# Kernel optimization log

Measured on AMD Instinct MI355X. Metric: run time of the kernel, lower is better.

## Reference

```python
import jax, jax.numpy as jnp
import numpy as np

N_MASTER = 100000
N_BOND = 200000
N_GLOB = 5000
E1 = 400000
E2 = 100000
D_IN = 64
D_OUT = 64
H = 4
SLOPE = 0.2  # leaky relu negative slope


def _mlp(x, W0, b0, W1, b1, W2):
    # LinearN with num_fc_layers=3: ELU, ELU, Identity (last layer no bias)
    h = jax.nn.elu(x @ W0 + b0)
    h = jax.nn.elu(h @ W1 + b1)
    return h @ W2  # (N, H*D_OUT)


def setup_inputs() -> dict:
    key = jax.random.key(0)
    ks = jax.random.split(key, 32)
    s = 0.1  # weight scale
    d = {
        "master_feats": jax.random.normal(ks[0], (N_MASTER, D_IN), jnp.float32),
        "bond_feats": jax.random.normal(ks[1], (N_BOND, D_IN), jnp.float32),
        "global_feats": jax.random.normal(ks[2], (N_GLOB, D_IN), jnp.float32),
        "atom_W0": jax.random.normal(ks[3], (D_IN, D_OUT), jnp.float32) * s,
        "atom_b0": jnp.zeros((D_OUT,), jnp.float32),
        "atom_W1": jax.random.normal(ks[4], (D_OUT, D_OUT), jnp.float32) * s,
        "atom_b1": jnp.zeros((D_OUT,), jnp.float32),
        "atom_W2": jax.random.normal(ks[5], (D_OUT, H * D_OUT), jnp.float32) * s,
        "bond_W0": jax.random.normal(ks[6], (D_IN, D_OUT), jnp.float32) * s,
        "bond_b0": jnp.zeros((D_OUT,), jnp.float32),
        "bond_W1": jax.random.normal(ks[7], (D_OUT, D_OUT), jnp.float32) * s,
        "bond_b1": jnp.zeros((D_OUT,), jnp.float32),
        "bond_W2": jax.random.normal(ks[8], (D_OUT, H * D_OUT), jnp.float32) * s,
        "glob_W0": jax.random.normal(ks[9], (D_IN, D_OUT), jnp.float32) * s,
        "glob_b0": jnp.zeros((D_OUT,), jnp.float32),
        "glob_W1": jax.random.normal(ks[10], (D_OUT, D_OUT), jnp.float32) * s,
        "glob_b1": jnp.zeros((D_OUT,), jnp.float32),
        "glob_W2": jax.random.normal(ks[11], (D_OUT, H * D_OUT), jnp.float32) * s,
        "attn_l": jax.random.normal(ks[12], (H, D_OUT), jnp.float32) * s,
        "attn_r": jax.random.normal(ks[13], (H, D_OUT), jnp.float32) * s,
        "e1_src": jax.random.randint(ks[14], (E1,), 0, N_BOND, jnp.int32),
        "e1_dst": jax.random.randint(ks[15], (E1,), 0, N_MASTER, jnp.int32),
        "e2_src": jax.random.randint(ks[16], (E2,), 0, N_GLOB, jnp.int32),
        "e2_dst": jax.random.randint(ks[17], (E2,), 0, N_MASTER, jnp.int32),
    }
    return d


def reference(master_feats, bond_feats, global_feats,
              atom_W0, atom_b0, atom_W1, atom_b1, atom_W2,
              bond_W0, bond_b0, bond_W1, bond_b1, bond_W2,
              glob_W0, glob_b0, glob_W1, glob_b1, glob_W2,
              attn_l, attn_r, e1_src, e1_dst, e2_src, e2_dst):
    # Per-node-type projections to (N, H, D_OUT)
    ft_m = _mlp(master_feats, atom_W0, atom_b0, atom_W1, atom_b1, atom_W2).reshape(N_MASTER, H, D_OUT)
    ft_b = _mlp(bond_feats, bond_W0, bond_b0, bond_W1, bond_b1, bond_W2).reshape(N_BOND, H, D_OUT)
    ft_g = _mlp(global_feats, glob_W0, glob_b0, glob_W1, glob_b1, glob_W2).reshape(N_GLOB, H, D_OUT)

    er = jnp.einsum('nhd,hd->nh', ft_m, attn_r)  # master (dst) scores
    el_b = jnp.einsum('nhd,hd->nh', ft_b, attn_l)
    el_g = jnp.einsum('nhd,hd->nh', ft_g, attn_l)

    # Per-edge logits: u_add_v then leaky relu
    e1 = jax.nn.leaky_relu(el_b[e1_src] + er[e1_dst], negative_slope=SLOPE)  # (E1, H)
    e2 = jax.nn.leaky_relu(el_g[e2_src] + er[e2_dst], negative_slope=SLOPE)  # (E2, H)

    # Joint edge softmax over all incoming edges per master node
    dst_all = jnp.concatenate([e1_dst, e2_dst])  # (E1+E2,)
    e_all = jnp.concatenate([e1, e2], axis=0)    # (E1+E2, H)
    emax = jax.ops.segment_max(e_all, dst_all, num_segments=N_MASTER)  # (N, H)
    ex = jnp.exp(e_all - emax[dst_all])
    esum = jax.ops.segment_sum(ex, dst_all, num_segments=N_MASTER)     # (N, H)
    a = ex / esum[dst_all]                                             # (E, H)

    # Aggregate: u_mul_e, sum per destination master node
    src_ft = jnp.concatenate([ft_b[e1_src], ft_g[e2_src]], axis=0)     # (E, H, D)
    msgs = src_ft * a[:, :, None]
    rst = jax.ops.segment_sum(msgs, dst_all, num_segments=N_MASTER)    # (N, H, D)
    return rst
```

## Files before the change

### kernel.cpp

```cpp
#include <hip/hip_runtime.h>

#define NM 100000
#define NB 200000
#define NG 5000
#define NE1 400000
#define NE2 100000
#define NE (NE1 + NE2)
#define NMP 100004
#define SCAN_BLOCKS 391

typedef __attribute__((ext_vector_type(8))) short bf16x8;
typedef __attribute__((ext_vector_type(4))) short short4v;
typedef __attribute__((ext_vector_type(4))) float f32x4;

__device__ __forceinline__ unsigned short f2bf(float f) {
    unsigned int u = __float_as_uint(f);
    u += 0x7FFFu + ((u >> 16) & 1u);
    return (unsigned short)(u >> 16);
}
__device__ __forceinline__ float bf2f(unsigned short u) {
    return __uint_as_float((unsigned int)u << 16);
}
__device__ __forceinline__ float elu_f(float x) {
    return x > 0.f ? x : __expf(x) - 1.f;
}
__device__ __forceinline__ char* swz(char* base, int j, int byteoff) {
    return base + j * 128 + ((((byteoff >> 4) ^ (j & 7)) << 4) | (byteoff & 15));
}

struct WEnt { const float* W; short* o; int I; int off; };
struct WAll { WEnt e[6]; };

__global__ __launch_bounds__(256) void wprep_all_kernel(WAll a)
{
    const int idx = blockIdx.x * 256 + threadIdx.x;
    #pragma unroll
    for (int j = 5; j >= 0; --j) {
        if (idx >= a.e[j].off) {
            const int local = idx - a.e[j].off;
            const int I = a.e[j].I;
            const int i = local >> 6, k = local & 63;
            a.e[j].o[local] = (short)f2bf(a.e[j].W[k * I + i]);
            break;
        }
    }
}

__global__ __launch_bounds__(256) void wt2prep_kernel(
    const float* __restrict__ W2b, const float* __restrict__ W2g,
    short* __restrict__ wt2)
{
    const int idx = blockIdx.x * 256 + threadIdx.x;
    const int i = idx >> 7, k = idx & 127;
    const float v = (k < 64) ? W2b[(k << 8) + i] : W2g[((k - 64) << 8) + i];
    wt2[idx] = (short)f2bf(v);
}

struct Eff3 { const float* W2[3]; const float* attn[3]; float* eff[3]; };
__global__ __launch_bounds__(256) void eff3_kernel(Eff3 a)
{
    const int b = blockIdx.x;
    const int t = threadIdx.x;
    const int h = t >> 6, k = t & 63;
    const float* wrow = a.W2[b] + (k << 8) + (h << 6);
    const float* arow = a.attn[b] + (h << 6);
    float s = 0.f;
    #pragma unroll 8
    for (int d = 0; d < 64; ++d) s = fmaf(wrow[d], arow[d], s);
    a.eff[b][(h << 6) + k] = s;
}

struct MlpArgs {
    const float* x[3]; int N[3];
    const short* W0t[3]; const float* b0[3];
    const short* W1t[3]; const float* b1[3];
    const float* eff[3];
    float* score[3];
    unsigned short* h2o[3];
    int bstart[3];
};

__global__ __launch_bounds__(256, 4) void mlp2_all_kernel(MlpArgs A)
{
    __shared__ __attribute__((aligned(128))) char ldsA[64 * 128];
    __shared__ __attribute__((aligned(128))) char ldsB[64 * 128];

    const int which = (blockIdx.x >= (unsigned)A.bstart[2]) ? 2
                    : (blockIdx.x >= (unsigned)A.bstart[1]) ? 1 : 0;
    const float* x = A.x[which];
    const int N = A.N[which];
    const short* W0t = A.W0t[which];
    const float* b0p = A.b0[which];
    const short* W1t = A.W1t[which];
    const float* b1p = A.b1[which];
    const float* eff = A.eff[which];
    float* score = A.score[which];
    unsigned short* h2p = A.h2o[which];

    const int tid = threadIdx.x;
    const int w = tid >> 6, l = tid & 63;
    const int g = l >> 4, c = l & 15;
    const int r0 = (blockIdx.x - A.bstart[which]) << 6;

    {
        const int j = tid >> 2, q = tid & 3;
        const int row = r0 + j;
        bf16x8 o0 = (bf16x8)0, o1 = (bf16x8)0;
        if (row < N) {
            const float4* xp = (const float4*)(x + ((size_t)row << 6) + (q << 4));
            #pragma unroll
            for (int u = 0; u < 2; ++u) {
                float4 v = xp[u];
                o0[u*4+0] = (short)f2bf(v.x); o0[u*4+1] = (short)f2bf(v.y);
                o0[u*4+2] = (short)f2bf(v.z); o0[u*4+3] = (short)f2bf(v.w);
            }
            #pragma unroll
            for (int u = 0; u < 2; ++u) {
                float4 v = xp[u + 2];
                o1[u*4+0] = (short)f2bf(v.x); o1[u*4+1] = (short)f2bf(v.y);
                o1[u*4+2] = (short)f2bf(v.z); o1[u*4+3] = (short)f2bf(v.w);
            }
        }
        *(bf16x8*)swz(ldsA, j, q * 32)      = o0;
        *(bf16x8*)swz(ldsA, j, q * 32 + 16) = o1;
    }
    __syncthreads();

    char* src = ldsA;
    char* dst = ldsB;
    #pragma unroll
    for (int layer = 0; layer < 2; ++layer) {
        const short* Wt = layer ? W1t : W0t;
        const float* bb = layer ? b1p : b0p;
        f32x4 acc[4] = {};
        #pragma unroll
        for (int step = 0; step < 2; ++step) {
            bf16x8 a = *(const bf16x8*)(Wt + (((16 * w + c) << 6) + 32 * step + 8 * g));
            #pragma unroll
            for (int t = 0; t < 4; ++t) {
                const int j = 16 * t + c;
                bf16x8 b = *(const bf16x8*)swz(src, j, 64 * step + 16 * g);
                acc[t] = __builtin_amdgcn_mfma_f32_16x16x32_bf16(a, b, acc[t], 0, 0, 0);
            }
        }
        const int i0 = 16 * w + 4 * g;
        const float4 bias = *(const float4*)(bb + i0);
        #pragma unroll
        for (int t = 0; t < 4; ++t) {
            const int j = 16 * t + c;
            short4v o;
            o[0] = (short)f2bf(elu_f(acc[t][0] + bias.x));
            o[1] = (short)f2bf(elu_f(acc[t][1] + bias.y));
            o[2] = (short)f2bf(elu_f(acc[t][2] + bias.z));
            o[3] = (short)f2bf(elu_f(acc[t][3] + bias.w));
            *(short4v*)swz(dst, j, 32 * w + 8 * g) = o;
        }
        __syncthreads();
        char* tmp = src; src = dst; dst = tmp;
    }

    {
        const int j = tid >> 2, h = tid & 3;
        const int row = r0 + j;
        float s = 0.f;
        #pragma unroll
        for (int c8 = 0; c8 < 8; ++c8) {
            bf16x8 v = *(const bf16x8*)swz(src, j, c8 * 16);
            const float4 e0 = *(const float4*)(eff + (h << 6) + (c8 << 3));
            const float4 e1 = *(const float4*)(eff + (h << 6) + (c8 << 3) + 4);
            s += bf2f((unsigned short)v[0]) * e0.x + bf2f((unsigned short)v[1]) * e0.y
               + bf2f((unsigned short)v[2]) * e0.z + bf2f((unsigned short)v[3]) * e0.w
               + bf2f((unsigned short)v[4]) * e1.x + bf2f((unsigned short)v[5]) * e1.y
               + bf2f((unsigned short)v[6]) * e1.z + bf2f((unsigned short)v[7]) * e1.w;
        }
        if (row < N) score[(row << 2) + h] = s;
    }

    if (h2p) {
        const int j = tid >> 2, q = tid & 3;
        const int row = r0 + j;
        if (row < N) {
            bf16x8 v0 = *(const bf16x8*)swz(src, j, q * 32);
            bf16x8 v1 = *(const bf16x8*)swz(src, j, q * 32 + 16);
            unsigned short* p = h2p + ((size_t)row << 6) + (q << 4);
            *(bf16x8*)p       = v0;
            *(bf16x8*)(p + 8) = v1;
        }
    }
}

__global__ void hist_kernel(const int* __restrict__ e1_dst,
                            const int* __restrict__ e2_dst,
                            int* __restrict__ counts)
{
    int i = blockIdx.x * blockDim.x + threadIdx.x;
    if (i < NE1) atomicAdd(&counts[e1_dst[i]], 1);
    else if (i < NE) atomicAdd(&counts[e2_dst[i - NE1]], 1);
}

__global__ __launch_bounds__(256) void scan1_kernel(
    const int* __restrict__ counts,
    int* __restrict__ prefix_inc,
    int* __restrict__ blocksums)
{
    const int i = blockIdx.x * 256 + threadIdx.x;
    const int lane = threadIdx.x & 63, wv = threadIdx.x >> 6;
    int v = (i < NM) ? counts[i] : 0;
    int x = v;
    #pragma unroll
    for (int o = 1; o < 64; o <<= 1) {
        int u = __shfl_up(x, o);
        if (lane >= o) x += u;
    }
    __shared__ int wsum[4];
    if (lane == 63) wsum[wv] = x;
    __syncthreads();
    int add = 0;
    #pragma unroll
    for (int k = 0; k < 3; ++k) add += (k < wv) ? wsum[k] : 0;
    x += add;
    if (i < NM) prefix_inc[i] = x;
    if (threadIdx.x == 255) blocksums[blockIdx.x] = x;
}

__global__ __launch_bounds__(512) void scan2_kernel(int* __restrict__ blocksums)
{
    const int t = threadIdx.x;
    const int lane = t & 63, wv = t >> 6;
    int v = (t < SCAN_BLOCKS) ? blocksums[t] : 0;
    int x = v;
    #pragma unroll
    for (int o = 1; o < 64; o <<= 1) {
        int u = __shfl_up(x, o);
        if (lane >= o) x += u;
    }
    __shared__ int wsum[8];
    if (lane == 63) wsum[wv] = x;
    __syncthreads();
    int add = 0;
    #pragma unroll
    for (int k = 0; k < 7; ++k) add += (k < wv) ? wsum[k] : 0;
    x += add;
    if (t < SCAN_BLOCKS) blocksums[t] = x - v;
}

__global__ __launch_bounds__(256) void scan3_kernel(
    const int* __restrict__ counts,
    const int* __restrict__ prefix_inc,
    const int* __restrict__ blocksums,
    int* __restrict__ offsets,
    int* __restrict__ cursor,
    int* __restrict__ cursor2)
{
    const int i = blockIdx.x * 256 + threadIdx.x;
    if (i > NM) return;
    if (i == NM) { offsets[NM] = NE; return; }
    const int off = prefix_inc[i] - counts[i] + blocksums[blockIdx.x];
    offsets[i] = off;
    cursor[i]  = off;
    cursor2[i] = off + counts[i];
}

__global__ void fill_kernel(const int* __restrict__ e1_src,
                            const int* __restrict__ e1_dst,
                            const int* __restrict__ e2_src,
                            const int* __restrict__ e2_dst,
                            const float* __restrict__ er,
                            const float* __restrict__ el_b,
                            const float* __restrict__ el_g,
                            int* __restrict__ cursor,
                            int* __restrict__ cursor2,
                            int* __restrict__ rows,
                            float4* __restrict__ expv)
{
    int i = blockIdx.x * blockDim.x + threadIdx.x;
    if (i >= NE) return;
    int dst, src, row, isglob;
    const float* el;
    if (i < NE1) { src = e1_src[i]; dst = e1_dst[i]; row = src;      el = el_b; isglob = 0; }
    else { int j = i - NE1; src = e2_src[j]; dst = e2_dst[j]; row = NB + src; el = el_g; isglob = 1; }
    const float4 l4 = *(const float4*)(el + (src << 2));
    const float4 r4 = *(const float4*)(er + (dst << 2));
    float4 v;
    v.x = l4.x + r4.x; v.x = v.x > 0.f ? v.x : 0.2f * v.x;
    v.y = l4.y + r4.y; v.y = v.y > 0.f ? v.y : 0.2f * v.y;
    v.z = l4.z + r4.z; v.z = v.z > 0.f ? v.z : 0.2f * v.z;
    v.w = l4.w + r4.w; v.w = v.w > 0.f ? v.w : 0.2f * v.w;
    float4 ev;
    ev.x = __expf(v.x); ev.y = __expf(v.y); ev.z = __expf(v.z); ev.w = __expf(v.w);
    int p = isglob ? (atomicSub(&cursor2[dst], 1) - 1)
                   : atomicAdd(&cursor[dst], 1);
    rows[p] = row;
    expv[p] = ev;
}

#define AGSTR 304
__global__ __launch_bounds__(1024) void aggregate_fused_kernel(
    const int* __restrict__ offsets,
    const int* __restrict__ split,
    const int* __restrict__ rows,
    const float* __restrict__ expv,
    const unsigned short* __restrict__ h2,
    const short* __restrict__ wt2,
    float* __restrict__ out)
{
    __shared__ __attribute__((aligned(16))) char agg_lds[64 * AGSTR];

    const int tid = threadIdx.x;
    const int wv = tid >> 6, l = tid & 63;
    const int h = l >> 4, c = l & 15;
    const int n0 = blockIdx.x << 4;

    {
        const int n = n0 + wv;
        const int start = offsets[n];
        const int sp    = split[n];
        const int end   = offsets[n + 1];

        f32x4 acc = {}, accg = {};
        float s = 0.f;

        for (int b = start; b < sp; b += 8) {
            const int rem = min(sp - b, 8);
            int row_l = 0; float v_l = 0.f;
            if (c < rem) { row_l = rows[b + c]; v_l = expv[((b + c) << 2) + h]; }
            short4v gv[8];
            #pragma unroll
            for (int e = 0; e < 8; ++e) {
                if (e < rem)
                    gv[e] = *(const short4v*)(h2 + ((size_t)__shfl(row_l, e) << 6) + (c << 2));
            }
            #pragma unroll
            for (int e = 0; e < 8; ++e) {
                if (e < rem) {
                    const float wgt = __shfl(v_l, (h << 4) + e);
                    s += wgt;
                    acc[0] = fmaf(bf2f((unsigned short)gv[e][0]), wgt, acc[0]);
                    acc[1] = fmaf(bf2f((unsigned short)gv[e][1]), wgt, acc[1]);
                    acc[2] = fmaf(bf2f((unsigned short)gv[e][2]), wgt, acc[2]);
                    acc[3] = fmaf(bf2f((unsigned short)gv[e][3]), wgt, acc[3]);
                }
            }
        }
        for (int b = sp; b < end; b += 8) {
            const int rem = min(end - b, 8);
            int row_l = 0; float v_l = 0.f;
            if (c < rem) { row_l = rows[b + c]; v_l = expv[((b + c) << 2) + h]; }
            short4v gv[8];
            #pragma unroll
            for (int e = 0; e < 8; ++e) {
                if (e < rem)
                    gv[e] = *(const short4v*)(h2 + ((size_t)__shfl(row_l, e) << 6) + (c << 2));
            }
            #pragma unroll
            for (int e = 0; e < 8; ++e) {
                if (e < rem) {
                    const float wgt = __shfl(v_l, (h << 4) + e);
                    s += wgt;
                    accg[0] = fmaf(bf2f((unsigned short)gv[e][0]), wgt, accg[0]);
                    accg[1] = fmaf(bf2f((unsigned short)gv[e][1]), wgt, accg[1]);
                    accg[2] = fmaf(bf2f((unsigned short)gv[e][2]), wgt, accg[2]);
                    accg[3] = fmaf(bf2f((unsigned short)gv[e][3]), wgt, accg[3]);
                }
            }
        }

        const float inv = (end > start) ? 1.f / s : 0.f;
        char* p = agg_lds + (h * 16 + wv) * AGSTR;
        short4v ob, og;
        ob[0] = (short)f2bf(acc[0] * inv);  ob[1] = (short)f2bf(acc[1] * inv);
        ob[2] = (short)f2bf(acc[2] * inv);  ob[3] = (short)f2bf(acc[3] * inv);
        og[0] = (short)f2bf(accg[0] * inv); og[1] = (short)f2bf(accg[1] * inv);
        og[2] = (short)f2bf(accg[2] * inv); og[3] = (short)f2bf(accg[3] * inv);
        *(short4v*)(p + 8 * c)       = ob;
        *(short4v*)(p + 128 + 8 * c) = og;
    }
    __syncthreads();

    {
        const int it = wv >> 2, hb = wv & 3;
        const int g = l >> 4;
        f32x4 oacc = {};
        #pragma unroll
        for (int st = 0; st < 4; ++st) {
            bf16x8 a = *(const bf16x8*)(wt2 + ((((hb << 6) + (it << 4) + c) << 7) + 32 * st + 8 * g));
            bf16x8 bfrag = *(const bf16x8*)(agg_lds + (hb * 16 + c) * AGSTR + 64 * st + 16 * g);
            oacc = __builtin_amdgcn_mfma_f32_16x16x32_bf16(a, bfrag, oacc, 0, 0, 0);
        }
        *(f32x4*)(out + ((size_t)(n0 + c) << 8) + (hb << 6) + (it << 4) + (g << 2)) = oacc;
    }
}

extern "C" void kernel_launch(void* const* d_in, const int* in_sizes, int n_in,
                              void* d_out, int out_size, void* d_ws, size_t ws_size,
                              hipStream_t stream)
{
    const float* master = (const float*)d_in[0];
    const float* bond   = (const float*)d_in[1];
    const float* glob   = (const float*)d_in[2];
    const float* aW0 = (const float*)d_in[3];
    const float* ab0 = (const float*)d_in[4];
    const float* aW1 = (const float*)d_in[5];
    const float* ab1 = (const float*)d_in[6];
    const float* aW2 = (const float*)d_in[7];
    const float* bW0 = (const float*)d_in[8];
    const float* bb0 = (const float*)d_in[9];
    const float* bW1 = (const float*)d_in[10];
    const float* bb1 = (const float*)d_in[11];
    const float* bW2 = (const float*)d_in[12];
    const float* gW0 = (const float*)d_in[13];
    const float* gb0 = (const float*)d_in[14];
    const float* gW1 = (const float*)d_in[15];
    const float* gb1 = (const float*)d_in[16];
    const float* gW2 = (const float*)d_in[17];
    const float* attn_l = (const float*)d_in[18];
    const float* attn_r = (const float*)d_in[19];
    const int* e1_src = (const int*)d_in[20];
    const int* e1_dst = (const int*)d_in[21];
    const int* e2_src = (const int*)d_in[22];
    const int* e2_dst = (const int*)d_in[23];
    float* out = (float*)d_out;

    unsigned short* h2 = (unsigned short*)d_ws;
    float* er   = (float*)(h2 + (size_t)(NB + NG) * 64);
    float* el_b = er + (size_t)NM * 4;
    float* el_g = el_b + (size_t)NB * 4;
    int* counts  = (int*)(el_g + (size_t)NG * 4);
    int* offsets = counts + NMP;
    int* cursor  = offsets + NMP;
    int* cursor2 = cursor + NMP;
    int* rows    = cursor2 + NMP;
    float4* expv = (float4*)(rows + NE);
    int* prefix_inc = (int*)(expv + NE);
    int* blocksums  = prefix_inc + NMP;
    float* effR  = (float*)(blocksums + 512);
    float* effLB = effR + 256;
    float* effLG = effLB + 256;
    short* wt2 = (short*)(effLG + 256);
    short* wtA = wt2 + 32768;
    short* wtB = wtA + 8192;
    short* wtG = wtB + 8192;

    hipMemsetAsync(counts, 0, sizeof(int) * NM, stream);

    WAll wa;
    wa.e[0] = {aW0, wtA,         64,     0};
    wa.e[1] = {aW1, wtA + 4096,  64,  4096};
    wa.e[2] = {bW0, wtB,         64,  8192};
    wa.e[3] = {bW1, wtB + 4096,  64, 12288};
    wa.e[4] = {gW0, wtG,         64, 16384};
    wa.e[5] = {gW1, wtG + 4096,  64, 20480};
    wprep_all_kernel<<<96, 256, 0, stream>>>(wa);
    wt2prep_kernel<<<128, 256, 0, stream>>>(bW2, gW2, wt2);
    Eff3 ef;
    ef.W2[0] = aW2; ef.attn[0] = attn_r; ef.eff[0] = effR;
    ef.W2[1] = bW2; ef.attn[1] = attn_l; ef.eff[1] = effLB;
    ef.W2[2] = gW2; ef.attn[2] = attn_l; ef.eff[2] = effLG;
    eff3_kernel<<<3, 256, 0, stream>>>(ef);

    MlpArgs ma;
    ma.x[0] = bond;   ma.N[0] = NB; ma.W0t[0] = wtB; ma.b0[0] = bb0;
    ma.W1t[0] = wtB + 4096; ma.b1[0] = bb1; ma.eff[0] = effLB;
    ma.score[0] = el_b; ma.h2o[0] = h2;
    ma.x[1] = glob;   ma.N[1] = NG; ma.W0t[1] = wtG; ma.b0[1] = gb0;
    ma.W1t[1] = wtG + 4096; ma.b1[1] = gb1; ma.eff[1] = effLG;
    ma.score[1] = el_g; ma.h2o[1] = h2 + (size_t)NB * 64;
    ma.x[2] = master; ma.N[2] = NM; ma.W0t[2] = wtA; ma.b0[2] = ab0;
    ma.W1t[2] = wtA + 4096; ma.b1[2] = ab1; ma.eff[2] = effR;
    ma.score[2] = er;   ma.h2o[2] = nullptr;
    ma.bstart[0] = 0;
    ma.bstart[1] = (NB + 63) / 64;
    ma.bstart[2] = ma.bstart[1] + (NG + 63) / 64;
    const int nblk = ma.bstart[2] + (NM + 63) / 64;
    mlp2_all_kernel<<<nblk, 256, 0, stream>>>(ma);

    hist_kernel<<<(NE + 255) / 256, 256, 0, stream>>>(e1_dst, e2_dst, counts);
    scan1_kernel<<<SCAN_BLOCKS, 256, 0, stream>>>(counts, prefix_inc, blocksums);
    scan2_kernel<<<1, 512, 0, stream>>>(blocksums);
    scan3_kernel<<<SCAN_BLOCKS + 1, 256, 0, stream>>>(counts, prefix_inc, blocksums,
                                                      offsets, cursor, cursor2);
    fill_kernel<<<(NE + 255) / 256, 256, 0, stream>>>(e1_src, e1_dst, e2_src, e2_dst,
                                                      er, el_b, el_g,
                                                      cursor, cursor2, rows, expv);
    aggregate_fused_kernel<<<NM / 16, 1024, 0, stream>>>(offsets, cursor2, rows,
                                                         (const float*)expv,
                                                         h2, wt2, out);
}
```

Before: 233.0 us.

## Shrink aggregate blocks to 256 threads with each wave handling four nodes

The aggregate kernel now launches 256-thread blocks in which each wave processes four destination nodes in sequence rather than one node per wave in 1024-thread blocks. The gather loop is restructured to load row indices and weights directly per lane in chunks of four edges with clamped indices, replacing the shuffle-based eight-edge batches. Each wave then runs four MFMA output tiles. The aim is better occupancy and scheduling flexibility with smaller blocks, and less shuffle overhead. The cost is redundant scalar loads across lanes, less memory-level parallelism per wave, and a padding offset added to the expv workspace.

```diff
diff --git a/kernel.cpp b/kernel.cpp
--- a/kernel.cpp
+++ b/kernel.cpp
@@ -295,7 +295,7 @@
 }
 
 #define AGSTR 304
-__global__ __launch_bounds__(1024) void aggregate_fused_kernel(
+__global__ __launch_bounds__(256) void aggregate_fused_kernel(
     const int* __restrict__ offsets,
     const int* __restrict__ split,
     const int* __restrict__ rows,
@@ -307,12 +307,14 @@
     __shared__ __attribute__((aligned(16))) char agg_lds[64 * AGSTR];
 
     const int tid = threadIdx.x;
-    const int wv = tid >> 6, l = tid & 63;
+    const int w = tid >> 6, l = tid & 63;
     const int h = l >> 4, c = l & 15;
     const int n0 = blockIdx.x << 4;
 
-    {
-        const int n = n0 + wv;
+    #pragma unroll
+    for (int j = 0; j < 4; ++j) {
+        const int ln = 4 * w + j;
+        const int n  = n0 + ln;
         const int start = offsets[n];
         const int sp    = split[n];
         const int end   = offsets[n + 1];
@@ -320,53 +322,51 @@
         f32x4 acc = {}, accg = {};
         float s = 0.f;
 
-        for (int b = start; b < sp; b += 8) {
-            const int rem = min(sp - b, 8);
-            int row_l = 0; float v_l = 0.f;
-            if (c < rem) { row_l = rows[b + c]; v_l = expv[((b + c) << 2) + h]; }
-            short4v gv[8];
-            #pragma unroll
-            for (int e = 0; e < 8; ++e) {
-                if (e < rem)
-                    gv[e] = *(const short4v*)(h2 + ((size_t)__shfl(row_l, e) << 6) + (c << 2));
-            }
-            #pragma unroll
-            for (int e = 0; e < 8; ++e) {
-                if (e < rem) {
-                    const float wgt = __shfl(v_l, (h << 4) + e);
-                    s += wgt;
-                    acc[0] = fmaf(bf2f((unsigned short)gv[e][0]), wgt, acc[0]);
-                    acc[1] = fmaf(bf2f((unsigned short)gv[e][1]), wgt, acc[1]);
-                    acc[2] = fmaf(bf2f((unsigned short)gv[e][2]), wgt, acc[2]);
-                    acc[3] = fmaf(bf2f((unsigned short)gv[e][3]), wgt, acc[3]);
-                }
-            }
-        }
-        for (int b = sp; b < end; b += 8) {
-            const int rem = min(end - b, 8);
-            int row_l = 0; float v_l = 0.f;
-            if (c < rem) { row_l = rows[b + c]; v_l = expv[((b + c) << 2) + h]; }
-            short4v gv[8];
-            #pragma unroll
-            for (int e = 0; e < 8; ++e) {
-                if (e < rem)
-                    gv[e] = *(const short4v*)(h2 + ((size_t)__shfl(row_l, e) << 6) + (c << 2));
-            }
-            #pragma unroll
-            for (int e = 0; e < 8; ++e) {
-                if (e < rem) {
-                    const float wgt = __shfl(v_l, (h << 4) + e);
-                    s += wgt;
-                    accg[0] = fmaf(bf2f((unsigned short)gv[e][0]), wgt, accg[0]);
-                    accg[1] = fmaf(bf2f((unsigned short)gv[e][1]), wgt, accg[1]);
-                    accg[2] = fmaf(bf2f((unsigned short)gv[e][2]), wgt, accg[2]);
-                    accg[3] = fmaf(bf2f((unsigned short)gv[e][3]), wgt, accg[3]);
-                }
+        for (int b = start; b < sp; b += 4) {
+            float  wg[4];
+            short4v gv[4];
+            #pragma unroll
+            for (int i = 0; i < 4; ++i) {
+                const int sl = b + i;
+                const int sc = sl < sp ? sl : sp - 1;
+                const float wv = expv[(sc << 2) + h];
+                wg[i] = (sl < sp) ? wv : 0.f;
+                const int row = rows[sc];
+                gv[i] = *(const short4v*)(h2 + ((size_t)row << 6) + (c << 2));
+            }
+            #pragma unroll
+            for (int i = 0; i < 4; ++i) {
+                s += wg[i];
+                acc[0] = fmaf(bf2f((unsigned short)gv[i][0]), wg[i], acc[0]);
+                acc[1] = fmaf(bf2f((unsigned short)gv[i][1]), wg[i], acc[1]);
+                acc[2] = fmaf(bf2f((unsigned short)gv[i][2]), wg[i], acc[2]);
+                acc[3] = fmaf(bf2f((unsigned short)gv[i][3]), wg[i], acc[3]);
+            }
+        }
+        for (int b = sp; b < end; b += 4) {
+            float  wg[4];
+            short4v gv[4];
+            #pragma unroll
+            for (int i = 0; i < 4; ++i) {
+                const int sl = b + i;
+                const int sc = sl < end ? sl : end - 1;
+                const float wv = expv[(sc << 2) + h];
+                wg[i] = (sl < end) ? wv : 0.f;
+                const int row = rows[sc];
+                gv[i] = *(const short4v*)(h2 + ((size_t)row << 6) + (c << 2));
+            }
+            #pragma unroll
+            for (int i = 0; i < 4; ++i) {
+                s += wg[i];
+                accg[0] = fmaf(bf2f((unsigned short)gv[i][0]), wg[i], accg[0]);
+                accg[1] = fmaf(bf2f((unsigned short)gv[i][1]), wg[i], accg[1]);
+                accg[2] = fmaf(bf2f((unsigned short)gv[i][2]), wg[i], accg[2]);
+                accg[3] = fmaf(bf2f((unsigned short)gv[i][3]), wg[i], accg[3]);
             }
         }
 
         const float inv = (end > start) ? 1.f / s : 0.f;
-        char* p = agg_lds + (h * 16 + wv) * AGSTR;
+        char* p = agg_lds + (h * 16 + ln) * AGSTR;
         short4v ob, og;
         ob[0] = (short)f2bf(acc[0] * inv);  ob[1] = (short)f2bf(acc[1] * inv);
         ob[2] = (short)f2bf(acc[2] * inv);  ob[3] = (short)f2bf(acc[3] * inv);
@@ -378,16 +378,18 @@
     __syncthreads();
 
     {
-        const int it = wv >> 2, hb = wv & 3;
         const int g = l >> 4;
-        f32x4 oacc = {};
         #pragma unroll
-        for (int st = 0; st < 4; ++st) {
-            bf16x8 a = *(const bf16x8*)(wt2 + ((((hb << 6) + (it << 4) + c) << 7) + 32 * st + 8 * g));
-            bf16x8 bfrag = *(const bf16x8*)(agg_lds + (hb * 16 + c) * AGSTR + 64 * st + 16 * g);
-            oacc = __builtin_amdgcn_mfma_f32_16x16x32_bf16(a, bfrag, oacc, 0, 0, 0);
-        }
-        *(f32x4*)(out + ((size_t)(n0 + c) << 8) + (hb << 6) + (it << 4) + (g << 2)) = oacc;
+        for (int it = 0; it < 4; ++it) {
+            f32x4 oacc = {};
+            #pragma unroll
+            for (int st = 0; st < 4; ++st) {
+                bf16x8 a = *(const bf16x8*)(wt2 + ((((w << 6) + (it << 4) + c) << 7) + 32 * st + 8 * g));
+                bf16x8 bfrag = *(const bf16x8*)(agg_lds + (w * 16 + c) * AGSTR + 64 * st + 16 * g);
+                oacc = __builtin_amdgcn_mfma_f32_16x16x32_bf16(a, bfrag, oacc, 0, 0, 0);
+            }
+            *(f32x4*)(out + ((size_t)(n0 + c) << 8) + (w << 6) + (it << 4) + (g << 2)) = oacc;
+        }
     }
 }
 
@@ -430,7 +432,7 @@
     int* cursor  = offsets + NMP;
     int* cursor2 = cursor + NMP;
     int* rows    = cursor2 + NMP;
-    float4* expv = (float4*)(rows + NE);
+    float4* expv = (float4*)(rows + NE + 16);
     int* prefix_inc = (int*)(expv + NE);
     int* blocksums  = prefix_inc + NMP;
     float* effR  = (float*)(blocksums + 512);
@@ -482,7 +484,7 @@
     fill_kernel<<<(NE + 255) / 256, 256, 0, stream>>>(e1_src, e1_dst, e2_src, e2_dst,
                                                       er, el_b, el_g,
                                                       cursor, cursor2, rows, expv);
-    aggregate_fused_kernel<<<NM / 16, 1024, 0, stream>>>(offsets, cursor2, rows,
-                                                         (const float*)expv,
-                                                         h2, wt2, out);
-}
+    aggregate_fused_kernel<<<NM / 16, 256, 0, stream>>>(offsets, cursor2, rows,
+                                                        (const float*)expv,
+                                                        h2, wt2, out);
+}
```

Measured after the change: 227.7 us. 2.2% less time.
